# Kernel tuning notes

Hardware: AMD Instinct MI355X
Metric: run time of the kernel (lower is better)

## Reference

```python
import jax, jax.numpy as jnp
import numpy as np
from jax import lax

K = 10  # k_neighbors (k = min(k, N); N=1024 so k=10)


def setup_inputs() -> dict:
    key = jax.random.key(0)
    ks = jax.random.split(key, 6)
    B, N, M, D = 4, 1024, 8, 128
    PROJ, NC, OUT = 64, 10, 128
    x = jax.random.normal(ks[0], (B, N, M, D), dtype=jnp.float32)
    # Linear params (torch stores weight as [out, in])
    W_proj_w = jax.random.normal(ks[1], (PROJ, D), dtype=jnp.float32) / np.sqrt(D)
    W_proj_b = jnp.zeros((PROJ,), dtype=jnp.float32)
    C = jax.random.normal(ks[2], (NC, PROJ), dtype=jnp.float32) * np.sqrt(2.0 / (NC + PROJ))
    Theta_w = jax.random.normal(ks[3], (OUT, D), dtype=jnp.float32) / np.sqrt(D)
    Theta_b = jnp.zeros((OUT,), dtype=jnp.float32)
    return {"x": x, "W_proj_w": W_proj_w, "W_proj_b": W_proj_b, "C": C,
            "Theta_w": Theta_w, "Theta_b": Theta_b}


def _forward(x, W_proj_w, W_proj_b, C, Theta_w, Theta_b):
    B, N, M, D = x.shape
    BM = B * M
    x_flat = jnp.transpose(x, (0, 2, 1, 3)).reshape(BM, N, D)
    Z = x_flat @ W_proj_w.T + W_proj_b  # [BM, N, P]
    # squared euclidean pairwise distances (same topk ordering as cdist)
    sq = jnp.sum(Z * Z, axis=-1)  # [BM, N]
    d2 = sq[:, :, None] + sq[:, None, :] - 2.0 * jnp.einsum('bnp,bmp->bnm', Z, Z)
    _, idx = lax.top_k(-d2, K)  # k smallest distances -> [BM, N, K]
    # scatter 1.0 at neighbor indices
    b_ix = jnp.arange(BM)[:, None, None]
    r_ix = jnp.arange(N)[None, :, None]
    H_knn = jnp.zeros((BM, N, N), dtype=jnp.float32).at[b_ix, r_ix, idx].set(1.0)
    H_cluster = jax.nn.softmax(Z @ C.T, axis=-1)  # [BM, N, NC]
    H = jnp.concatenate([H_knn, H_cluster], axis=-1)  # [BM, N, N+NC]
    # hypergraph conv with degree normalization
    D_e = H.sum(axis=1)  # [BM, E]
    D_e_inv = jnp.where(D_e > 0, 1.0 / jnp.maximum(D_e, 1e-12), 0.0)
    D_v = H.sum(axis=2)  # [BM, N]
    D_v_inv_sqrt = jnp.where(D_v > 0, 1.0 / jnp.sqrt(jnp.maximum(D_v, 1e-12)), 0.0)
    X_trans = x_flat @ Theta_w.T + Theta_b  # [BM, N, F]
    out = D_v_inv_sqrt[:, :, None] * X_trans
    out = jnp.einsum('bne,bnf->bef', H, out)   # H^T @ out
    out = D_e_inv[:, :, None] * out
    out = jnp.einsum('bne,bef->bnf', H, out)   # H @ out
    out = D_v_inv_sqrt[:, :, None] * out
    out = jax.nn.elu(out)
    return jnp.transpose(out.reshape(B, M, N, -1), (0, 2, 1, 3))  # [B, N, M, F]


def reference(x, W_proj_w, W_proj_b, C, Theta_w, Theta_b):
    return _forward(x, W_proj_w, W_proj_b, C, Theta_w, Theta_b)
```

## Files before the change

### kernel.cpp

```cpp
#include <hip/hip_runtime.h>
#include <hip/hip_bf16.h>
#include <cstdint>
#include <cstddef>

#define BMC 32
#define NNODE 1024
#define DIN 128
#define PPROJ 64
#define NCLUS 10
#define FOUT 128
#define KNB 10

typedef _Float16 half8 __attribute__((ext_vector_type(8)));
typedef float f32x4 __attribute__((ext_vector_type(4)));

static const size_t OFF_Z    = 0;
static const size_t OFF_SQ   = 2097152;
static const size_t OFF_HC   = 2129920;
static const size_t OFF_IDX  = 2457600;
static const size_t OFF_CNT  = 2785280;
static const size_t OFF_FILL = 2818048;
static const size_t OFF_EC   = 2850816;
static const size_t OFF_DCV  = 2891776;
static const size_t OFF_OFFS = 2892096;
static const size_t OFF_ADJ  = 2924864;
static const size_t OFF_FLAG = 3252544;
static const size_t OFF_END  = 3252608;
static const size_t OFF_WPH  = OFF_FILL;
static const size_t OFF_WPL  = OFF_FILL +  4096;
static const size_t OFF_THH  = OFF_FILL +  8192;
static const size_t OFF_THL  = OFF_FILL + 16384;

__device__ __forceinline__ float bfu(unsigned int lo16) {
    return __uint_as_float(lo16 << 16);
}
__device__ __forceinline__ float bfhi(unsigned int w) {
    return __uint_as_float(w & 0xffff0000u);
}
__device__ __forceinline__ float ldf(const void* p, size_t i, bool isbf) {
    return isbf ? bfu((unsigned int)((const unsigned short*)p)[i])
                : ((const float*)p)[i];
}
__device__ __forceinline__ unsigned short f2bf(float v) {
    __hip_bfloat16 h = __float2bfloat16(v);
    return *(unsigned short*)&h;
}

__device__ __forceinline__ unsigned long long mkkey(float v, int col) {
    unsigned int bits = __float_as_uint(v);
    unsigned int s = bits ^ (0x80000000u | (unsigned int)((int)bits >> 31));
    return ((unsigned long long)s << 32) | (unsigned int)col;
}
__device__ __forceinline__ void kcas(unsigned long long &a, unsigned long long &b) {
    bool c = b < a;
    unsigned long long t = c ? b : a;
    b = c ? a : b;
    a = t;
}
__device__ __forceinline__ void kmin(unsigned long long &a, unsigned long long b) {
    a = (b < a) ? b : a;
}

__global__ __launch_bounds__(256) void k_split(const unsigned int* __restrict__ xw,
                                               const void* __restrict__ Wp,
                                               const void* __restrict__ Th,
                                               int* __restrict__ flag,
                                               _Float16* __restrict__ WpH,
                                               _Float16* __restrict__ WpL,
                                               _Float16* __restrict__ ThH,
                                               _Float16* __restrict__ ThL,
                                               int* __restrict__ cntz,
                                               float* __restrict__ EcZ) {
    __shared__ int red[256];
    int t = threadIdx.x;
    int c = 0;
    for (int i = t; i < 1024; i += 256) {
        float b = bfu(xw[i] & 0xffffu);
        float ab = fabsf(b);
        if (ab > 9.5e-7f && ab < 1.0e6f) c++;
    }
    red[t] = c;
    __syncthreads();
    for (int off = 128; off > 0; off >>= 1) {
        if (t < off) red[t] += red[t + off];
        __syncthreads();
    }
    const bool isbf = (red[0] >= 700);
    if (blockIdx.x == 0 && t == 0) flag[0] = isbf ? 1 : 0;

    int i = blockIdx.x * 256 + t;
    cntz[i] = 0;
    if (i < 8192) cntz[i + 24576] = 0;
    EcZ[i] = 0.0f;
    if (i < 16704) EcZ[i + 24576] = 0.0f;

    if (i < 8192) {
        float v = ldf(Wp, i, isbf);
        _Float16 h = (_Float16)v;
        WpH[i] = h;
        WpL[i] = (_Float16)((v - (float)h) * 2048.0f);
    } else {
        int j = i - 8192;
        float v = ldf(Th, j, isbf);
        _Float16 h = (_Float16)v;
        ThH[j] = h;
        ThL[j] = (_Float16)((v - (float)h) * 2048.0f);
    }
}

__global__ __launch_bounds__(256) void k_proj(const void* __restrict__ x,
                                              const _Float16* __restrict__ WpH,
                                              const _Float16* __restrict__ WpL,
                                              const void* __restrict__ Wpb,
                                              const void* __restrict__ Cm,
                                              const int* __restrict__ flag,
                                              _Float16* __restrict__ Zh,
                                              _Float16* __restrict__ Zl,
                                              float* __restrict__ sqv,
                                              float* __restrict__ Hc) {
    __shared__ __align__(16) _Float16 wps[2][64][72];
    __shared__ __align__(16) _Float16 xsh[2][32][72];
    __shared__ float zs[32][68];
    __shared__ float cs[10][64];

    const bool isbf = (flag[0] != 0);
    int tid = threadIdx.x;
    int bi  = blockIdx.x;
    int bm  = bi >> 5;
    int n0  = (bi & 31) << 5;
    int b   = bm >> 3, m = bm & 7;

    int lane = tid & 63, wave = tid >> 6;
    int m16 = lane & 15, quad = lane >> 4;
    int rh = wave >> 1, ch = wave & 1;

    for (int e = tid; e < 640; e += 256) cs[e >> 6][e & 63] = ldf(Cm, e, isbf);

    f32x4 aH[2], aX[2];
#pragma unroll
    for (int t = 0; t < 2; ++t) {
        aH[t] = (f32x4){0.f, 0.f, 0.f, 0.f};
        aX[t] = (f32x4){0.f, 0.f, 0.f, 0.f};
    }

    for (int kc = 0; kc < 2; ++kc) {
        __syncthreads();
        for (int e = tid; e < 512; e += 256) {
            int p = e >> 3, c = e & 7;
            *(uint4*)&wps[0][p][c * 8] =
                *(const uint4*)(WpH + (size_t)p * 128 + kc * 64 + c * 8);
            *(uint4*)&wps[1][p][c * 8] =
                *(const uint4*)(WpL + (size_t)p * 128 + kc * 64 + c * 8);
        }
        for (int e = tid; e < 2048; e += 256) {
            int r = e >> 6, dk = e & 63;
            float v = ldf(x, (((size_t)b * NNODE + n0 + r) * 8 + m) * DIN + kc * 64 + dk, isbf);
            _Float16 h = (_Float16)v;
            xsh[0][r][dk] = h;
            xsh[1][r][dk] = (_Float16)((v - (float)h) * 2048.0f);
        }
        __syncthreads();
#pragma unroll
        for (int c32 = 0; c32 < 2; ++c32) {
            half8 Ah = *(const half8*)&xsh[0][rh * 16 + m16][c32 * 32 + quad * 8];
            half8 Al = *(const half8*)&xsh[1][rh * 16 + m16][c32 * 32 + quad * 8];
#pragma unroll
            for (int t = 0; t < 2; ++t) {
                int p = ch * 32 + t * 16 + m16;
                half8 Bh = *(const half8*)&wps[0][p][c32 * 32 + quad * 8];
                half8 Bl = *(const half8*)&wps[1][p][c32 * 32 + quad * 8];
                aH[t] = __builtin_amdgcn_mfma_f32_16x16x32_f16(Ah, Bh, aH[t], 0, 0, 0);
                aX[t] = __builtin_amdgcn_mfma_f32_16x16x32_f16(Al, Bh, aX[t], 0, 0, 0);
                aX[t] = __builtin_amdgcn_mfma_f32_16x16x32_f16(Ah, Bl, aX[t], 0, 0, 0);
            }
        }
    }

#pragma unroll
    for (int t = 0; t < 2; ++t) {
        int p = ch * 32 + t * 16 + m16;
        float bias = ldf(Wpb, p, isbf);
#pragma unroll
        for (int r = 0; r < 4; ++r) {
            int row = rh * 16 + quad * 4 + r;
            float v = aH[t][r] + aX[t][r] * (1.0f / 2048.0f) + bias;
            zs[row][p] = v;
            size_t off = ((size_t)bm * NNODE + n0 + row) * 64 + p;
            _Float16 h = (_Float16)v;
            Zh[off] = h;
            Zl[off] = (_Float16)((v - (float)h) * 2048.0f);
        }
    }
    __syncthreads();

    int row = tid >> 3, slot = tid & 7;
    int d0 = slot * 8;
    float sp = 0.f;
#pragma unroll
    for (int dd = 0; dd < 8; ++dd) { float z = zs[row][d0+dd]; sp += z * z; }
#pragma unroll
    for (int mm = 1; mm < 8; mm <<= 1) sp += __shfl_xor(sp, mm, 8);
    size_t g = (size_t)bm * NNODE + n0 + row;
    if (slot == 0) sqv[g] = sp;

    float sc[10];
#pragma unroll
    for (int c = 0; c < 10; ++c) {
        float pa = 0.f;
#pragma unroll
        for (int dd = 0; dd < 8; ++dd) pa += zs[row][d0+dd] * cs[c][d0+dd];
#pragma unroll
        for (int mm = 1; mm < 8; mm <<= 1) pa += __shfl_xor(pa, mm, 8);
        sc[c] = pa;
    }
    float mx = sc[0];
#pragma unroll
    for (int c = 1; c < 10; ++c) mx = fmaxf(mx, sc[c]);
    float ssum = 0.f;
#pragma unroll
    for (int c = 0; c < 10; ++c) { sc[c] = expf(sc[c] - mx); ssum += sc[c]; }
    float inv = 1.0f / ssum;
#pragma unroll
    for (int c = 0; c < 10; ++c)
        if ((c & 7) == slot) Hc[g * 10 + c] = sc[c] * inv;
}

__global__ __launch_bounds__(256) void k_theta(const void* __restrict__ x,
                                               const _Float16* __restrict__ ThH,
                                               const _Float16* __restrict__ ThL,
                                               const void* __restrict__ Thb,
                                               const int* __restrict__ flag,
                                               float* __restrict__ Xt) {
    __shared__ __align__(16) _Float16 ths[2][128][72];
    __shared__ __align__(16) _Float16 xsh[32][72];

    const bool isbf = (flag[0] != 0);
    int tid = threadIdx.x;
    int bi  = blockIdx.x;
    int bm  = bi >> 5;
    int n0  = (bi & 31) << 5;
    int b   = bm >> 3, m = bm & 7;

    int lane = tid & 63, wave = tid >> 6;
    int m16 = lane & 15, quad = lane >> 4;
    int rh = wave >> 1, ch = wave & 1;

    f32x4 aH[4], aX[4];
#pragma unroll
    for (int t = 0; t < 4; ++t) {
        aH[t] = (f32x4){0.f, 0.f, 0.f, 0.f};
        aX[t] = (f32x4){0.f, 0.f, 0.f, 0.f};
    }

    for (int kc = 0; kc < 2; ++kc) {
        __syncthreads();
        for (int e = tid; e < 1024; e += 256) {
            int f = e >> 3, c = e & 7;
            *(uint4*)&ths[0][f][c * 8] =
                *(const uint4*)(ThH + (size_t)f * 128 + kc * 64 + c * 8);
            *(uint4*)&ths[1][f][c * 8] =
                *(const uint4*)(ThL + (size_t)f * 128 + kc * 64 + c * 8);
        }
        for (int e = tid; e < 2048; e += 256) {
            int r = e >> 6, dk = e & 63;
            float v = ldf(x, (((size_t)b * NNODE + n0 + r) * 8 + m) * DIN + kc * 64 + dk, isbf);
            xsh[r][dk] = (_Float16)v;
        }
        __syncthreads();
#pragma unroll
        for (int c32 = 0; c32 < 2; ++c32) {
            half8 Ah = *(const half8*)&xsh[rh * 16 + m16][c32 * 32 + quad * 8];
#pragma unroll
            for (int t = 0; t < 4; ++t) {
                int f = ch * 64 + t * 16 + m16;
                half8 Bh = *(const half8*)&ths[0][f][c32 * 32 + quad * 8];
                half8 Bl = *(const half8*)&ths[1][f][c32 * 32 + quad * 8];
                aH[t] = __builtin_amdgcn_mfma_f32_16x16x32_f16(Ah, Bh, aH[t], 0, 0, 0);
                aX[t] = __builtin_amdgcn_mfma_f32_16x16x32_f16(Ah, Bl, aX[t], 0, 0, 0);
            }
        }
    }
#pragma unroll
    for (int t = 0; t < 4; ++t) {
        int f = ch * 64 + t * 16 + m16;
        float bias = ldf(Thb, f, isbf);
        size_t rb = (size_t)bm * NNODE + n0 + rh * 16 + quad * 4;
#pragma unroll
        for (int r = 0; r < 4; ++r) {
            Xt[(rb + r) * 128 + f] = aH[t][r] + aX[t][r] * (1.0f / 2048.0f) + bias;
        }
    }
}

#define TOPK_SELECT(J0)                                                        \
  {                                                                            \
    unsigned long long b0 = mkkey(ST[(sslot     ) * 36 + srow], (J0) + sslot);        \
    unsigned long long b1 = mkkey(ST[(sslot +  8) * 36 + srow], (J0) + sslot + 8);    \
    unsigned long long b2 = mkkey(ST[(sslot + 16) * 36 + srow], (J0) + sslot + 16);   \
    unsigned long long b3 = mkkey(ST[(sslot + 24) * 36 + srow], (J0) + sslot + 24);   \
    unsigned long long b4 = mkkey(ST[(sslot + 32) * 36 + srow], (J0) + sslot + 32);   \
    unsigned long long b5 = mkkey(ST[(sslot + 40) * 36 + srow], (J0) + sslot + 40);   \
    unsigned long long b6 = mkkey(ST[(sslot + 48) * 36 + srow], (J0) + sslot + 48);   \
    unsigned long long b7 = mkkey(ST[(sslot + 56) * 36 + srow], (J0) + sslot + 56);   \
    kcas(b0, b1); kcas(b2, b3); kcas(b4, b5); kcas(b6, b7);                    \
    kcas(b0, b2); kcas(b1, b3); kcas(b4, b6); kcas(b5, b7);                    \
    kcas(b1, b2); kcas(b5, b6);                                                \
    kcas(b0, b4); kcas(b1, b5); kcas(b2, b6); kcas(b3, b7);                    \
    kcas(b2, b4); kcas(b3, b5);                                                \
    kcas(b1, b2); kcas(b3, b4); kcas(b5, b6);                                  \
    kmin(keys[2], b7); kmin(keys[3], b6); kmin(keys[4], b5); kmin(keys[5], b4);\
    kmin(keys[6], b3); kmin(keys[7], b2); kmin(keys[8], b1); kmin(keys[9], b0);\
    kcas(keys[0], keys[8]); kcas(keys[1], keys[9]);                            \
    kcas(keys[2], keys[6]); kcas(keys[3], keys[7]);                            \
    kcas(keys[4], keys[8]); kcas(keys[5], keys[9]);                            \
    kcas(keys[2], keys[4]); kcas(keys[3], keys[5]);                            \
    kcas(keys[6], keys[8]); kcas(keys[7], keys[9]);                            \
    kcas(keys[0], keys[1]); kcas(keys[2], keys[3]);                            \
    kcas(keys[4], keys[5]); kcas(keys[6], keys[7]); kcas(keys[8], keys[9]);    \
  }

#define TOPK_TILE(J0, CH0,CH1,CL0,CL1,CSQ, NH0,NH1,NL0,NL1,NSQ)                \
  {                                                                            \
    f32x4 acc  = {0.f, 0.f, 0.f, 0.f};                                         \
    f32x4 accx = {0.f, 0.f, 0.f, 0.f};                                         \
    acc  = __builtin_amdgcn_mfma_f32_16x16x32_f16(ah0, CH0, acc, 0, 0, 0);     \
    acc  = __builtin_amdgcn_mfma_f32_16x16x32_f16(ah1, CH1, acc, 0, 0, 0);     \
    accx = __builtin_amdgcn_mfma_f32_16x16x32_f16(al0, CH0, accx, 0, 0, 0);    \
    accx = __builtin_amdgcn_mfma_f32_16x16x32_f16(ah0, CL0, accx, 0, 0, 0);    \
    accx = __builtin_amdgcn_mfma_f32_16x16x32_f16(al1, CH1, accx, 0, 0, 0);    \
    accx = __builtin_amdgcn_mfma_f32_16x16x32_f16(ah1, CL1, accx, 0, 0, 0);    \
    f32x4 sc;                                                                  \
    _Pragma("unroll")                                                          \
    for (int r = 0; r < 4; ++r) {                                              \
      float g = acc[r] + accx[r] * (1.0f / 2048.0f);                           \
      sc[r] = fmaf(-2.0f, g, CSQ);                                             \
    }                                                                          \
    *(f32x4*)&ST[cl * 36 + quad * 4] = sc;                                     \
    f32x4 accB  = {0.f, 0.f, 0.f, 0.f};                                        \
    f32x4 accxB = {0.f, 0.f, 0.f, 0.f};                                        \
    accB  = __builtin_amdgcn_mfma_f32_16x16x32_f16(ah0b, CH0, accB, 0, 0, 0);  \
    accB  = __builtin_amdgcn_mfma_f32_16x16x32_f16(ah1b, CH1, accB, 0, 0, 0);  \
    accxB = __builtin_amdgcn_mfma_f32_16x16x32_f16(al0b, CH0, accxB, 0, 0, 0); \
    accxB = __builtin_amdgcn_mfma_f32_16x16x32_f16(ah0b, CL0, accxB, 0, 0, 0); \
    accxB = __builtin_amdgcn_mfma_f32_16x16x32_f16(al1b, CH1, accxB, 0, 0, 0); \
    accxB = __builtin_amdgcn_mfma_f32_16x16x32_f16(ah1b, CL1, accxB, 0, 0, 0); \
    _Pragma("unroll")                                                          \
    for (int r = 0; r < 4; ++r) {                                              \
      float g = accB[r] + accxB[r] * (1.0f / 2048.0f);                         \
      sc[r] = fmaf(-2.0f, g, CSQ);                                             \
    }                                                                          \
    *(f32x4*)&ST[cl * 36 + 16 + quad * 4] = sc;                                \
    {                                                                          \
      const _Float16* pnb = Zhb + (size_t)((J0) + 64 + cl) * 64 + quad * 8;    \
      const _Float16* pnl = Zlb + (size_t)((J0) + 64 + cl) * 64 + quad * 8;    \
      NH0 = *(const half8*)pnb;                                                \
      NH1 = *(const half8*)(pnb + 32);                                         \
      NL0 = *(const half8*)pnl;                                                \
      NL1 = *(const half8*)(pnl + 32);                                         \
      NSQ = sqb[(J0) + 64 + cl];                                               \
    }                                                                          \
    asm volatile("s_waitcnt lgkmcnt(0)" ::: "memory");                         \
    __builtin_amdgcn_s_barrier();                                              \
    asm volatile("" ::: "memory");                                             \
    TOPK_SELECT(J0);                                                           \
    asm volatile("" ::: "memory");                                             \
    __builtin_amdgcn_s_barrier();                                              \
    asm volatile("" ::: "memory");                                             \
  }

__global__ __launch_bounds__(256) void k_topk(const _Float16* __restrict__ Zh,
                                              const _Float16* __restrict__ Zl,
                                              const float* __restrict__ sqv,
                                              int* __restrict__ idxo,
                                              int* __restrict__ cnt) {
    __shared__ float ST[64 * 36];

    int tid = threadIdx.x;
    int bi  = blockIdx.x;
    int bm  = bi >> 5;
    int n0  = (bi & 31) << 5;
    const _Float16* Zhb = Zh + (size_t)bm * NNODE * 64;
    const _Float16* Zlb = Zl + (size_t)bm * NNODE * 64;
    const float*    sqb = sqv + (size_t)bm * NNODE;

    int lane = tid & 63, wave = tid >> 6;
    int m16 = lane & 15, quad = lane >> 4;
    int cl = wave * 16 + m16;

    half8 ah0, ah1, al0, al1, ah0b, ah1b, al0b, al1b;
    {
        size_t ab = (size_t)(n0 + m16) * 64 + quad * 8;
        ah0 = *(const half8*)(Zhb + ab);
        ah1 = *(const half8*)(Zhb + ab + 32);
        al0 = *(const half8*)(Zlb + ab);
        al1 = *(const half8*)(Zlb + ab + 32);
        size_t ab2 = ab + 16 * 64;
        ah0b = *(const half8*)(Zhb + ab2);
        ah1b = *(const half8*)(Zhb + ab2 + 32);
        al0b = *(const half8*)(Zlb + ab2);
        al1b = *(const half8*)(Zlb + ab2 + 32);
    }

    unsigned long long keys[10];
#pragma unroll
    for (int j = 0; j < 10; ++j) keys[j] = ~0ULL;

    int srow  = tid >> 3;
    int sslot = tid & 7;

    half8 cbh0, cbh1, cbl0, cbl1, nbh0, nbh1, nbl0, nbl1;
    float csq, nsq;
    {
        const _Float16* pb = Zhb + (size_t)cl * 64 + quad * 8;
        const _Float16* pl = Zlb + (size_t)cl * 64 + quad * 8;
        cbh0 = *(const half8*)pb;
        cbh1 = *(const half8*)(pb + 32);
        cbl0 = *(const half8*)pl;
        cbl1 = *(const half8*)(pl + 32);
        csq  = sqb[cl];
    }

    for (int tp = 0; tp < 8; ++tp) {
        int j0a = tp << 7;
        TOPK_TILE(j0a,      cbh0, cbh1, cbl0, cbl1, csq, nbh0, nbh1, nbl0, nbl1, nsq)
        TOPK_TILE(j0a + 64, nbh0, nbh1, nbl0, nbl1, nsq, cbh0, cbh1, cbl0, cbl1, csq)
    }

    size_t gr = (size_t)bm * NNODE + n0 + srow;
    for (int it = 0; it < 10; ++it) {
        unsigned long long mine = keys[0];
        unsigned long long best = mine;
#pragma unroll
        for (int mm = 1; mm < 8; mm <<= 1) {
            unsigned long long o = __shfl_xor(best, mm, 8);
            if (o < best) best = o;
        }
        if (best == mine) {
#pragma unroll
            for (int j = 0; j < 9; ++j) keys[j] = keys[j+1];
            keys[9] = ~0ULL;
            int col = (int)(best & 0xFFFFFFFFu);
            idxo[gr * KNB + it] = col;
            atomicAdd(&cnt[bm * NNODE + col], 1);
        }
    }
}
#undef TOPK_TILE
#undef TOPK_SELECT

__global__ __launch_bounds__(256) void k_csr(const int* __restrict__ cnt,
                                             const int* __restrict__ idxb,
                                             int* __restrict__ offs,
                                             int* __restrict__ adj) {
    __shared__ int part[256];
    __shared__ int fillL[1024];
    int bm = blockIdx.x, t = threadIdx.x;
    int base = bm * 1024 + t * 4;
    int c0 = cnt[base], c1 = cnt[base+1], c2 = cnt[base+2], c3 = cnt[base+3];
    int ps = c0 + c1 + c2 + c3;
    part[t] = ps;
    __syncthreads();
    for (int off = 1; off < 256; off <<= 1) {
        int add = (t >= off) ? part[t - off] : 0;
        __syncthreads();
        part[t] += add;
        __syncthreads();
    }
    int e0 = part[t] - ps;
    int gb = bm * (NNODE * KNB);
    int o0 = gb + e0, o1 = o0 + c0, o2 = o1 + c1, o3 = o2 + c2;
    offs[base]   = o0;
    offs[base+1] = o1;
    offs[base+2] = o2;
    offs[base+3] = o3;
    fillL[t*4]   = o0;
    fillL[t*4+1] = o1;
    fillL[t*4+2] = o2;
    fillL[t*4+3] = o3;
    __syncthreads();
    int ibase = bm * (NNODE * KNB);
    for (int e = t; e < NNODE * KNB; e += 256) {
        int eidx = idxb[ibase + e];
        int pos = atomicAdd(&fillL[eidx], 1);
        adj[pos] = (bm << 10) + (e / 10);
    }
}

__global__ __launch_bounds__(256) void k_edgeclus(const float* __restrict__ Xt,
                                                  const int* __restrict__ offs,
                                                  const int* __restrict__ cnt,
                                                  const int* __restrict__ adj,
                                                  unsigned short* __restrict__ Ek,
                                                  const float* __restrict__ Hc,
                                                  float* __restrict__ Ec,
                                                  float* __restrict__ Dcv) {
    __shared__ float hcs[128][12];
    int tid = threadIdx.x;
    int bi  = blockIdx.x;

    if (bi < 256) {
        int bm = bi >> 3;
        int ch = bi & 7;
        int n0 = ch * 128;

        for (int e = tid; e < 1280; e += 256) {
            int r = e / 10, c = e - r * 10;
            hcs[r][c] = Hc[((size_t)bm * NNODE + n0 + r) * 10 + c];
        }
        __syncthreads();

        int f = tid & 127;
        int h = tid >> 7;
        int c0 = h * 5;
        float acc[5]  = {0.f,0.f,0.f,0.f,0.f};
        float dacc[5] = {0.f,0.f,0.f,0.f,0.f};
#pragma unroll 2
        for (int n = 0; n < 128; ++n) {
            float xv = Xt[((size_t)bm * NNODE + n0 + n) * 128 + f];
#pragma unroll
            for (int j = 0; j < 5; ++j) {
                float hv = hcs[n][c0 + j];
                acc[j]  = fmaf(hv, xv, acc[j]);
                dacc[j] += hv;
            }
        }
#pragma unroll
        for (int j = 0; j < 5; ++j)
            atomicAdd(&Ec[((size_t)bm * 10 + c0 + j) * 128 + f], acc[j]);
        if (f == 0) {
#pragma unroll
            for (int j = 0; j < 5; ++j) atomicAdd(&Dcv[bm * 10 + c0 + j], dacc[j]);
        }
        return;
    }

    int ebi = bi - 256;
    int swz = (ebi & 7) * 512 + (ebi >> 3);
    int e = swz * 8 + (tid >> 5);
    int l = tid & 31;
    int start = offs[e];
    int num = cnt[e];
    float4 acc = {0.f, 0.f, 0.f, 0.f};
    if (num > 0) {
        int nm1 = num - 1;
        int gidx[16];
#pragma unroll
        for (int j = 0; j < 16; ++j) {
            int jj = (j < nm1) ? j : nm1;
            gidx[j] = adj[start + jj];
        }
#pragma unroll
        for (int j = 0; j < 16; ++j) {
            float4 a = *(const float4*)(Xt + (size_t)gidx[j] * 128 + l * 4);
            float w = (j < num) ? 1.0f : 0.0f;
            acc.x = fmaf(w, a.x, acc.x);
            acc.y = fmaf(w, a.y, acc.y);
            acc.z = fmaf(w, a.z, acc.z);
            acc.w = fmaf(w, a.w, acc.w);
        }
        int i = 16;
        for (; i + 1 < num; i += 2) {
            int g0 = adj[start + i];
            int g1 = adj[start + i + 1];
            float4 a = *(const float4*)(Xt + (size_t)g0 * 128 + l * 4);
            float4 b = *(const float4*)(Xt + (size_t)g1 * 128 + l * 4);
            acc.x += a.x + b.x; acc.y += a.y + b.y;
            acc.z += a.z + b.z; acc.w += a.w + b.w;
        }
        if (i < num) {
            int g0 = adj[start + i];
            float4 a = *(const float4*)(Xt + (size_t)g0 * 128 + l * 4);
            acc.x += a.x; acc.y += a.y; acc.z += a.z; acc.w += a.w;
        }
    }
    float scale = (num > 0) ? 1.0f / (float)num : 0.0f;
    ushort4 o;
    o.x = f2bf(acc.x * scale);
    o.y = f2bf(acc.y * scale);
    o.z = f2bf(acc.z * scale);
    o.w = f2bf(acc.w * scale);
    *(ushort4*)(Ek + (size_t)e * 128 + l * 4) = o;
}

__global__ __launch_bounds__(256) void k_final(const unsigned short* __restrict__ Ek,
                                               const float* __restrict__ Ec,
                                               const float* __restrict__ Hc,
                                               const float* __restrict__ Dcv,
                                               const int* __restrict__ idxb,
                                               float* __restrict__ out) {
    int tid = threadIdx.x;
    int bi  = blockIdx.x;
    int swz = (bi & 7) * 512 + (bi >> 3);
    int g = swz * 8 + (tid >> 5);
    int l = tid & 31;
    int bm = g >> 10, n = g & 1023;
    const int* ip = idxb + (size_t)g * 10;
    const unsigned short* ekb = Ek + ((size_t)bm << 10) * 128 + l * 4;

    int e0 = ip[0], e1 = ip[1], e2 = ip[2], e3 = ip[3], e4 = ip[4];
    int e5 = ip[5], e6 = ip[6], e7 = ip[7], e8 = ip[8], e9 = ip[9];
    ushort4 u0 = *(const ushort4*)(ekb + (size_t)e0 * 128);
    ushort4 u1 = *(const ushort4*)(ekb + (size_t)e1 * 128);
    ushort4 u2 = *(const ushort4*)(ekb + (size_t)e2 * 128);
    ushort4 u3 = *(const ushort4*)(ekb + (size_t)e3 * 128);
    ushort4 u4 = *(const ushort4*)(ekb + (size_t)e4 * 128);
    ushort4 u5 = *(const ushort4*)(ekb + (size_t)e5 * 128);
    ushort4 u6 = *(const ushort4*)(ekb + (size_t)e6 * 128);
    ushort4 u7 = *(const ushort4*)(ekb + (size_t)e7 * 128);
    ushort4 u8 = *(const ushort4*)(ekb + (size_t)e8 * 128);
    ushort4 u9 = *(const ushort4*)(ekb + (size_t)e9 * 128);

    float4 acc;
    acc.x = bfu(u0.x) + bfu(u1.x) + bfu(u2.x) + bfu(u3.x) + bfu(u4.x)
          + bfu(u5.x) + bfu(u6.x) + bfu(u7.x) + bfu(u8.x) + bfu(u9.x);
    acc.y = bfu(u0.y) + bfu(u1.y) + bfu(u2.y) + bfu(u3.y) + bfu(u4.y)
          + bfu(u5.y) + bfu(u6.y) + bfu(u7.y) + bfu(u8.y) + bfu(u9.y);
    acc.z = bfu(u0.z) + bfu(u1.z) + bfu(u2.z) + bfu(u3.z) + bfu(u4.z)
          + bfu(u5.z) + bfu(u6.z) + bfu(u7.z) + bfu(u8.z) + bfu(u9.z);
    acc.w = bfu(u0.w) + bfu(u1.w) + bfu(u2.w) + bfu(u3.w) + bfu(u4.w)
          + bfu(u5.w) + bfu(u6.w) + bfu(u7.w) + bfu(u8.w) + bfu(u9.w);

    const float* hp  = Hc + (size_t)g * 10;
    const float* dcp = Dcv + (size_t)bm * 10;
    const float* ecp = Ec + (size_t)bm * 10 * 128 + l * 4;
#pragma unroll
    for (int c = 0; c < 10; ++c) {
        float d  = dcp[c];
        float hv = (d > 0.f) ? hp[c] / d : 0.f;
        float4 ec = *(const float4*)(ecp + c * 128);
        acc.x += hv * ec.x; acc.y += hv * ec.y;
        acc.z += hv * ec.z; acc.w += hv * ec.w;
    }
    float4 r;
    r.x = acc.x * (1.0f / 11.0f);
    r.y = acc.y * (1.0f / 11.0f);
    r.z = acc.z * (1.0f / 11.0f);
    r.w = acc.w * (1.0f / 11.0f);
    r.x = (r.x > 0.f) ? r.x : expm1f(r.x);
    r.y = (r.y > 0.f) ? r.y : expm1f(r.y);
    r.z = (r.z > 0.f) ? r.z : expm1f(r.z);
    r.w = (r.w > 0.f) ? r.w : expm1f(r.w);
    int b = bm >> 3, m = bm & 7;
    *(float4*)(out + (((size_t)b * NNODE + n) * 8 + m) * 128 + l * 4) = r;
}

extern "C" void kernel_launch(void* const* d_in, const int* in_sizes, int n_in,
                              void* d_out, int out_size, void* d_ws, size_t ws_size,
                              hipStream_t stream) {
    const void* x   = d_in[0];
    const void* Wp  = d_in[1];
    const void* Wpb = d_in[2];
    const void* Cm  = d_in[3];
    const void* Th  = d_in[4];
    const void* Thb = d_in[5];
    float* ws = (float*)d_ws;

    if (ws_size < OFF_END * sizeof(float)) return;

    _Float16* Zh = (_Float16*)(ws + OFF_Z);
    _Float16* Zl = (_Float16*)(ws + OFF_Z + 1048576);
    float* sqv  = ws + OFF_SQ;
    float* Hc   = ws + OFF_HC;
    int*   idxb = (int*)(ws + OFF_IDX);
    int*   cnt  = (int*)(ws + OFF_CNT);
    float* Ec   = ws + OFF_EC;
    float* Dcv  = ws + OFF_DCV;
    int*   offs = (int*)(ws + OFF_OFFS);
    int*   adj  = (int*)(ws + OFF_ADJ);
    int*   flag = (int*)(ws + OFF_FLAG);
    _Float16* WpH = (_Float16*)(ws + OFF_WPH);
    _Float16* WpL = (_Float16*)(ws + OFF_WPL);
    _Float16* ThH = (_Float16*)(ws + OFF_THH);
    _Float16* ThL = (_Float16*)(ws + OFF_THL);
    unsigned short* Ek = (unsigned short*)(ws + OFF_Z);
    float* Xt  = (float*)d_out;
    float* out = (float*)d_out;

    k_split   <<<96,   256, 0, stream>>>((const unsigned int*)x, Wp, Th, flag,
                                         WpH, WpL, ThH, ThL, cnt, Ec);
    k_proj    <<<1024, 256, 0, stream>>>(x, WpH, WpL, Wpb, Cm, flag, Zh, Zl, sqv, Hc);
    k_topk    <<<1024, 256, 0, stream>>>(Zh, Zl, sqv, idxb, cnt);
    k_csr     <<<32,   256, 0, stream>>>(cnt, idxb, offs, adj);
    k_theta   <<<1024, 256, 0, stream>>>(x, ThH, ThL, Thb, flag, Xt);
    k_edgeclus<<<4352, 256, 0, stream>>>(Xt, offs, cnt, adj, Ek, Hc, Ec, Dcv);
    k_final   <<<4096, 256, 0, stream>>>(Ek, Ec, Hc, Dcv, idxb, out);
}
```

Before: 252.1 us.

## Split top-k over column halves with merge kernel; fuse CSR build into theta

The k-nearest-neighbour search is split so that each row's 1024 candidate columns are scanned by two blocks of 512 columns each, doubling the grid. Each block writes its local top-10 as packed keys into scratch space in the output buffer. A new merge kernel combines the two sorted lists with a min/compare-swap network, then writes the indices and neighbour counts. The small 32-block CSR construction is moved into extra blocks of the theta projection kernel so it no longer runs as its own serialized launch. This trades an extra pass over the partial results for more parallelism in the dominant top-k stage.

```diff
diff --git a/kernel.cpp b/kernel.cpp
--- a/kernel.cpp
+++ b/kernel.cpp
@@ -33,9 +33,6 @@
 
 __device__ __forceinline__ float bfu(unsigned int lo16) {
     return __uint_as_float(lo16 << 16);
-}
-__device__ __forceinline__ float bfhi(unsigned int w) {
-    return __uint_as_float(w & 0xffff0000u);
 }
 __device__ __forceinline__ float ldf(const void* p, size_t i, bool isbf) {
     return isbf ? bfu((unsigned int)((const unsigned short*)p)[i])
@@ -223,73 +220,6 @@
 #pragma unroll
     for (int c = 0; c < 10; ++c)
         if ((c & 7) == slot) Hc[g * 10 + c] = sc[c] * inv;
-}
-
-__global__ __launch_bounds__(256) void k_theta(const void* __restrict__ x,
-                                               const _Float16* __restrict__ ThH,
-                                               const _Float16* __restrict__ ThL,
-                                               const void* __restrict__ Thb,
-                                               const int* __restrict__ flag,
-                                               float* __restrict__ Xt) {
-    __shared__ __align__(16) _Float16 ths[2][128][72];
-    __shared__ __align__(16) _Float16 xsh[32][72];
-
-    const bool isbf = (flag[0] != 0);
-    int tid = threadIdx.x;
-    int bi  = blockIdx.x;
-    int bm  = bi >> 5;
-    int n0  = (bi & 31) << 5;
-    int b   = bm >> 3, m = bm & 7;
-
-    int lane = tid & 63, wave = tid >> 6;
-    int m16 = lane & 15, quad = lane >> 4;
-    int rh = wave >> 1, ch = wave & 1;
-
-    f32x4 aH[4], aX[4];
-#pragma unroll
-    for (int t = 0; t < 4; ++t) {
-        aH[t] = (f32x4){0.f, 0.f, 0.f, 0.f};
-        aX[t] = (f32x4){0.f, 0.f, 0.f, 0.f};
-    }
-
-    for (int kc = 0; kc < 2; ++kc) {
-        __syncthreads();
-        for (int e = tid; e < 1024; e += 256) {
-            int f = e >> 3, c = e & 7;
-            *(uint4*)&ths[0][f][c * 8] =
-                *(const uint4*)(ThH + (size_t)f * 128 + kc * 64 + c * 8);
-            *(uint4*)&ths[1][f][c * 8] =
-                *(const uint4*)(ThL + (size_t)f * 128 + kc * 64 + c * 8);
-        }
-        for (int e = tid; e < 2048; e += 256) {
-            int r = e >> 6, dk = e & 63;
-            float v = ldf(x, (((size_t)b * NNODE + n0 + r) * 8 + m) * DIN + kc * 64 + dk, isbf);
-            xsh[r][dk] = (_Float16)v;
-        }
-        __syncthreads();
-#pragma unroll
-        for (int c32 = 0; c32 < 2; ++c32) {
-            half8 Ah = *(const half8*)&xsh[rh * 16 + m16][c32 * 32 + quad * 8];
-#pragma unroll
-            for (int t = 0; t < 4; ++t) {
-                int f = ch * 64 + t * 16 + m16;
-                half8 Bh = *(const half8*)&ths[0][f][c32 * 32 + quad * 8];
-                half8 Bl = *(const half8*)&ths[1][f][c32 * 32 + quad * 8];
-                aH[t] = __builtin_amdgcn_mfma_f32_16x16x32_f16(Ah, Bh, aH[t], 0, 0, 0);
-                aX[t] = __builtin_amdgcn_mfma_f32_16x16x32_f16(Ah, Bl, aX[t], 0, 0, 0);
-            }
-        }
-    }
-#pragma unroll
-    for (int t = 0; t < 4; ++t) {
-        int f = ch * 64 + t * 16 + m16;
-        float bias = ldf(Thb, f, isbf);
-        size_t rb = (size_t)bm * NNODE + n0 + rh * 16 + quad * 4;
-#pragma unroll
-        for (int r = 0; r < 4; ++r) {
-            Xt[(rb + r) * 128 + f] = aH[t][r] + aX[t][r] * (1.0f / 2048.0f) + bias;
-        }
-    }
 }
 
 #define TOPK_SELECT(J0)                                                        \
@@ -371,14 +301,16 @@
 __global__ __launch_bounds__(256) void k_topk(const _Float16* __restrict__ Zh,
                                               const _Float16* __restrict__ Zl,
                                               const float* __restrict__ sqv,
-                                              int* __restrict__ idxo,
-                                              int* __restrict__ cnt) {
+                                              unsigned long long* __restrict__ pk) {
     __shared__ float ST[64 * 36];
 
     int tid = threadIdx.x;
     int bi  = blockIdx.x;
-    int bm  = bi >> 5;
-    int n0  = (bi & 31) << 5;
+    int bm  = bi >> 6;
+    int rem = bi & 63;
+    int n0   = (rem & 31) << 5;
+    int half = rem >> 5;
+    int cb   = half << 9;
     const _Float16* Zhb = Zh + (size_t)bm * NNODE * 64;
     const _Float16* Zlb = Zl + (size_t)bm * NNODE * 64;
     const float*    sqb = sqv + (size_t)bm * NNODE;
@@ -411,22 +343,22 @@
     half8 cbh0, cbh1, cbl0, cbl1, nbh0, nbh1, nbl0, nbl1;
     float csq, nsq;
     {
-        const _Float16* pb = Zhb + (size_t)cl * 64 + quad * 8;
-        const _Float16* pl = Zlb + (size_t)cl * 64 + quad * 8;
+        const _Float16* pb = Zhb + (size_t)(cb + cl) * 64 + quad * 8;
+        const _Float16* pl = Zlb + (size_t)(cb + cl) * 64 + quad * 8;
         cbh0 = *(const half8*)pb;
         cbh1 = *(const half8*)(pb + 32);
         cbl0 = *(const half8*)pl;
         cbl1 = *(const half8*)(pl + 32);
-        csq  = sqb[cl];
-    }
-
-    for (int tp = 0; tp < 8; ++tp) {
-        int j0a = tp << 7;
+        csq  = sqb[cb + cl];
+    }
+
+    for (int tp = 0; tp < 4; ++tp) {
+        int j0a = cb + (tp << 7);
         TOPK_TILE(j0a,      cbh0, cbh1, cbl0, cbl1, csq, nbh0, nbh1, nbl0, nbl1, nsq)
         TOPK_TILE(j0a + 64, nbh0, nbh1, nbl0, nbl1, nsq, cbh0, cbh1, cbl0, cbl1, csq)
     }
 
-    size_t gr = (size_t)bm * NNODE + n0 + srow;
+    size_t pr = ((size_t)bm * NNODE + n0 + srow) * 20 + (size_t)half * 10;
     for (int it = 0; it < 10; ++it) {
         unsigned long long mine = keys[0];
         unsigned long long best = mine;
@@ -439,50 +371,153 @@
 #pragma unroll
             for (int j = 0; j < 9; ++j) keys[j] = keys[j+1];
             keys[9] = ~0ULL;
-            int col = (int)(best & 0xFFFFFFFFu);
-            idxo[gr * KNB + it] = col;
-            atomicAdd(&cnt[bm * NNODE + col], 1);
+            pk[pr + it] = best;
         }
     }
 }
 #undef TOPK_TILE
 #undef TOPK_SELECT
 
-__global__ __launch_bounds__(256) void k_csr(const int* __restrict__ cnt,
-                                             const int* __restrict__ idxb,
-                                             int* __restrict__ offs,
-                                             int* __restrict__ adj) {
+__global__ __launch_bounds__(256) void k_merge(const unsigned long long* __restrict__ pk,
+                                               int* __restrict__ idxo,
+                                               int* __restrict__ cnt) {
+    int r = blockIdx.x * 256 + threadIdx.x;
+    const unsigned long long* p = pk + (size_t)r * 20;
+    unsigned long long a0 = p[0], a1 = p[1], a2 = p[2], a3 = p[3], a4 = p[4];
+    unsigned long long a5 = p[5], a6 = p[6], a7 = p[7], a8 = p[8], a9 = p[9];
+    unsigned long long b0 = p[10], b1 = p[11], b2 = p[12], b3 = p[13], b4 = p[14];
+    unsigned long long b5 = p[15], b6 = p[16], b7 = p[17], b8 = p[18], b9 = p[19];
+
+    kmin(a0, b9); kmin(a1, b8); kmin(a2, b7); kmin(a3, b6); kmin(a4, b5);
+    kmin(a5, b4); kmin(a6, b3); kmin(a7, b2); kmin(a8, b1); kmin(a9, b0);
+
+    kcas(a0, a8); kcas(a1, a9);
+    kcas(a2, a6); kcas(a3, a7);
+    kcas(a4, a8); kcas(a5, a9);
+    kcas(a2, a4); kcas(a3, a5);
+    kcas(a6, a8); kcas(a7, a9);
+    kcas(a0, a1); kcas(a2, a3);
+    kcas(a4, a5); kcas(a6, a7); kcas(a8, a9);
+
+    int bm = r >> 10;
+    int* cb = cnt + (bm << 10);
+    int* ip = idxo + (size_t)r * 10;
+    int c0 = (int)(a0 & 0xFFFFFFFFu); ip[0] = c0; atomicAdd(&cb[c0], 1);
+    int c1 = (int)(a1 & 0xFFFFFFFFu); ip[1] = c1; atomicAdd(&cb[c1], 1);
+    int c2 = (int)(a2 & 0xFFFFFFFFu); ip[2] = c2; atomicAdd(&cb[c2], 1);
+    int c3 = (int)(a3 & 0xFFFFFFFFu); ip[3] = c3; atomicAdd(&cb[c3], 1);
+    int c4 = (int)(a4 & 0xFFFFFFFFu); ip[4] = c4; atomicAdd(&cb[c4], 1);
+    int c5 = (int)(a5 & 0xFFFFFFFFu); ip[5] = c5; atomicAdd(&cb[c5], 1);
+    int c6 = (int)(a6 & 0xFFFFFFFFu); ip[6] = c6; atomicAdd(&cb[c6], 1);
+    int c7 = (int)(a7 & 0xFFFFFFFFu); ip[7] = c7; atomicAdd(&cb[c7], 1);
+    int c8 = (int)(a8 & 0xFFFFFFFFu); ip[8] = c8; atomicAdd(&cb[c8], 1);
+    int c9 = (int)(a9 & 0xFFFFFFFFu); ip[9] = c9; atomicAdd(&cb[c9], 1);
+}
+
+__global__ __launch_bounds__(256) void k_thetacsr(const void* __restrict__ x,
+                                                  const _Float16* __restrict__ ThH,
+                                                  const _Float16* __restrict__ ThL,
+                                                  const void* __restrict__ Thb,
+                                                  const int* __restrict__ flag,
+                                                  float* __restrict__ Xt,
+                                                  const int* __restrict__ cnt,
+                                                  const int* __restrict__ idxb,
+                                                  int* __restrict__ offs,
+                                                  int* __restrict__ adj) {
+    __shared__ __align__(16) _Float16 ths[2][128][72];
+    __shared__ __align__(16) _Float16 xsh[32][72];
     __shared__ int part[256];
     __shared__ int fillL[1024];
-    int bm = blockIdx.x, t = threadIdx.x;
-    int base = bm * 1024 + t * 4;
-    int c0 = cnt[base], c1 = cnt[base+1], c2 = cnt[base+2], c3 = cnt[base+3];
-    int ps = c0 + c1 + c2 + c3;
-    part[t] = ps;
-    __syncthreads();
-    for (int off = 1; off < 256; off <<= 1) {
-        int add = (t >= off) ? part[t - off] : 0;
+
+    int tid = threadIdx.x;
+    if (blockIdx.x < 32) {
+        int bm = blockIdx.x, t = tid;
+        int base = bm * 1024 + t * 4;
+        int c0 = cnt[base], c1 = cnt[base+1], c2 = cnt[base+2], c3 = cnt[base+3];
+        int ps = c0 + c1 + c2 + c3;
+        part[t] = ps;
         __syncthreads();
-        part[t] += add;
+        for (int off = 1; off < 256; off <<= 1) {
+            int add = (t >= off) ? part[t - off] : 0;
+            __syncthreads();
+            part[t] += add;
+            __syncthreads();
+        }
+        int e0 = part[t] - ps;
+        int gb = bm * (NNODE * KNB);
+        int o0 = gb + e0, o1 = o0 + c0, o2 = o1 + c1, o3 = o2 + c2;
+        offs[base]   = o0;
+        offs[base+1] = o1;
+        offs[base+2] = o2;
+        offs[base+3] = o3;
+        fillL[t*4]   = o0;
+        fillL[t*4+1] = o1;
+        fillL[t*4+2] = o2;
+        fillL[t*4+3] = o3;
         __syncthreads();
-    }
-    int e0 = part[t] - ps;
-    int gb = bm * (NNODE * KNB);
-    int o0 = gb + e0, o1 = o0 + c0, o2 = o1 + c1, o3 = o2 + c2;
-    offs[base]   = o0;
-    offs[base+1] = o1;
-    offs[base+2] = o2;
-    offs[base+3] = o3;
-    fillL[t*4]   = o0;
-    fillL[t*4+1] = o1;
-    fillL[t*4+2] = o2;
-    fillL[t*4+3] = o3;
-    __syncthreads();
-    int ibase = bm * (NNODE * KNB);
-    for (int e = t; e < NNODE * KNB; e += 256) {
-        int eidx = idxb[ibase + e];
-        int pos = atomicAdd(&fillL[eidx], 1);
-        adj[pos] = (bm << 10) + (e / 10);
+        int ibase = bm * (NNODE * KNB);
+        for (int e = t; e < NNODE * KNB; e += 256) {
+            int eidx = idxb[ibase + e];
+            int pos = atomicAdd(&fillL[eidx], 1);
+            adj[pos] = (bm << 10) + (e / 10);
+        }
+        return;
+    }
+
+    const bool isbf = (flag[0] != 0);
+    int bi  = blockIdx.x - 32;
+    int bm  = bi >> 5;
+    int n0  = (bi & 31) << 5;
+    int b   = bm >> 3, m = bm & 7;
+
+    int lane = tid & 63, wave = tid >> 6;
+    int m16 = lane & 15, quad = lane >> 4;
+    int rh = wave >> 1, ch = wave & 1;
+
+    f32x4 aH[4], aX[4];
+#pragma unroll
+    for (int t = 0; t < 4; ++t) {
+        aH[t] = (f32x4){0.f, 0.f, 0.f, 0.f};
+        aX[t] = (f32x4){0.f, 0.f, 0.f, 0.f};
+    }
+
+    for (int kc = 0; kc < 2; ++kc) {
+        __syncthreads();
+        for (int e = tid; e < 1024; e += 256) {
+            int f = e >> 3, c = e & 7;
+            *(uint4*)&ths[0][f][c * 8] =
+                *(const uint4*)(ThH + (size_t)f * 128 + kc * 64 + c * 8);
+            *(uint4*)&ths[1][f][c * 8] =
+                *(const uint4*)(ThL + (size_t)f * 128 + kc * 64 + c * 8);
+        }
+        for (int e = tid; e < 2048; e += 256) {
+            int r = e >> 6, dk = e & 63;
+            float v = ldf(x, (((size_t)b * NNODE + n0 + r) * 8 + m) * DIN + kc * 64 + dk, isbf);
+            xsh[r][dk] = (_Float16)v;
+        }
+        __syncthreads();
+#pragma unroll
+        for (int c32 = 0; c32 < 2; ++c32) {
+            half8 Ah = *(const half8*)&xsh[rh * 16 + m16][c32 * 32 + quad * 8];
+#pragma unroll
+            for (int t = 0; t < 4; ++t) {
+                int f = ch * 64 + t * 16 + m16;
+                half8 Bh = *(const half8*)&ths[0][f][c32 * 32 + quad * 8];
+                half8 Bl = *(const half8*)&ths[1][f][c32 * 32 + quad * 8];
+                aH[t] = __builtin_amdgcn_mfma_f32_16x16x32_f16(Ah, Bh, aH[t], 0, 0, 0);
+                aX[t] = __builtin_amdgcn_mfma_f32_16x16x32_f16(Ah, Bl, aX[t], 0, 0, 0);
+            }
+        }
+    }
+#pragma unroll
+    for (int t = 0; t < 4; ++t) {
+        int f = ch * 64 + t * 16 + m16;
+        float bias = ldf(Thb, f, isbf);
+        size_t rb = (size_t)bm * NNODE + n0 + rh * 16 + quad * 4;
+#pragma unroll
+        for (int r = 0; r < 4; ++r) {
+            Xt[(rb + r) * 128 + f] = aH[t][r] + aX[t][r] * (1.0f / 2048.0f) + bias;
+        }
     }
 }
 
@@ -673,15 +708,16 @@
     _Float16* ThH = (_Float16*)(ws + OFF_THH);
     _Float16* ThL = (_Float16*)(ws + OFF_THL);
     unsigned short* Ek = (unsigned short*)(ws + OFF_Z);
+    unsigned long long* pk = (unsigned long long*)d_out;
     float* Xt  = (float*)d_out;
     float* out = (float*)d_out;
 
     k_split   <<<96,   256, 0, stream>>>((const unsigned int*)x, Wp, Th, flag,
                                          WpH, WpL, ThH, ThL, cnt, Ec);
     k_proj    <<<1024, 256, 0, stream>>>(x, WpH, WpL, Wpb, Cm, flag, Zh, Zl, sqv, Hc);
-    k_topk    <<<1024, 256, 0, stream>>>(Zh, Zl, sqv, idxb, cnt);
-    k_csr     <<<32,   256, 0, stream>>>(cnt, idxb, offs, adj);
-    k_theta   <<<1024, 256, 0, stream>>>(x, ThH, ThL, Thb, flag, Xt);
+    k_topk    <<<2048, 256, 0, stream>>>(Zh, Zl, sqv, pk);
+    k_merge   <<<128,  256, 0, stream>>>(pk, idxb, cnt);
+    k_thetacsr<<<1056, 256, 0, stream>>>(x, ThH, ThL, Thb, flag, Xt, cnt, idxb, offs, adj);
     k_edgeclus<<<4352, 256, 0, stream>>>(Xt, offs, cnt, adj, Ek, Hc, Ec, Dcv);
     k_final   <<<4096, 256, 0, stream>>>(Ek, Ec, Hc, Dcv, idxb, out);
 }
```

After: 259.5 us. 3.0% more time.

## Merge top-k and theta projection into one interleaved launch

Applied to the files above, without the earlier changes.

Combines the independent k_topk and k_theta kernels into a single launch of 2048 blocks, where even blocks do the kNN top-k selection and odd blocks compute the Theta projection. The aim is to overlap the compute-bound top-k work with the memory-heavy theta GEMM and remove one launch. Shared memory becomes a union sized for the larger branch, which may lower occupancy for the top-k blocks.

```diff
diff --git a/kernel.cpp b/kernel.cpp
--- a/kernel.cpp
+++ b/kernel.cpp
@@ -33,9 +33,6 @@
 
 __device__ __forceinline__ float bfu(unsigned int lo16) {
     return __uint_as_float(lo16 << 16);
-}
-__device__ __forceinline__ float bfhi(unsigned int w) {
-    return __uint_as_float(w & 0xffff0000u);
 }
 __device__ __forceinline__ float ldf(const void* p, size_t i, bool isbf) {
     return isbf ? bfu((unsigned int)((const unsigned short*)p)[i])
@@ -223,73 +220,6 @@
 #pragma unroll
     for (int c = 0; c < 10; ++c)
         if ((c & 7) == slot) Hc[g * 10 + c] = sc[c] * inv;
-}
-
-__global__ __launch_bounds__(256) void k_theta(const void* __restrict__ x,
-                                               const _Float16* __restrict__ ThH,
-                                               const _Float16* __restrict__ ThL,
-                                               const void* __restrict__ Thb,
-                                               const int* __restrict__ flag,
-                                               float* __restrict__ Xt) {
-    __shared__ __align__(16) _Float16 ths[2][128][72];
-    __shared__ __align__(16) _Float16 xsh[32][72];
-
-    const bool isbf = (flag[0] != 0);
-    int tid = threadIdx.x;
-    int bi  = blockIdx.x;
-    int bm  = bi >> 5;
-    int n0  = (bi & 31) << 5;
-    int b   = bm >> 3, m = bm & 7;
-
-    int lane = tid & 63, wave = tid >> 6;
-    int m16 = lane & 15, quad = lane >> 4;
-    int rh = wave >> 1, ch = wave & 1;
-
-    f32x4 aH[4], aX[4];
-#pragma unroll
-    for (int t = 0; t < 4; ++t) {
-        aH[t] = (f32x4){0.f, 0.f, 0.f, 0.f};
-        aX[t] = (f32x4){0.f, 0.f, 0.f, 0.f};
-    }
-
-    for (int kc = 0; kc < 2; ++kc) {
-        __syncthreads();
-        for (int e = tid; e < 1024; e += 256) {
-            int f = e >> 3, c = e & 7;
-            *(uint4*)&ths[0][f][c * 8] =
-                *(const uint4*)(ThH + (size_t)f * 128 + kc * 64 + c * 8);
-            *(uint4*)&ths[1][f][c * 8] =
-                *(const uint4*)(ThL + (size_t)f * 128 + kc * 64 + c * 8);
-        }
-        for (int e = tid; e < 2048; e += 256) {
-            int r = e >> 6, dk = e & 63;
-            float v = ldf(x, (((size_t)b * NNODE + n0 + r) * 8 + m) * DIN + kc * 64 + dk, isbf);
-            xsh[r][dk] = (_Float16)v;
-        }
-        __syncthreads();
-#pragma unroll
-        for (int c32 = 0; c32 < 2; ++c32) {
-            half8 Ah = *(const half8*)&xsh[rh * 16 + m16][c32 * 32 + quad * 8];
-#pragma unroll
-            for (int t = 0; t < 4; ++t) {
-                int f = ch * 64 + t * 16 + m16;
-                half8 Bh = *(const half8*)&ths[0][f][c32 * 32 + quad * 8];
-                half8 Bl = *(const half8*)&ths[1][f][c32 * 32 + quad * 8];
-                aH[t] = __builtin_amdgcn_mfma_f32_16x16x32_f16(Ah, Bh, aH[t], 0, 0, 0);
-                aX[t] = __builtin_amdgcn_mfma_f32_16x16x32_f16(Ah, Bl, aX[t], 0, 0, 0);
-            }
-        }
-    }
-#pragma unroll
-    for (int t = 0; t < 4; ++t) {
-        int f = ch * 64 + t * 16 + m16;
-        float bias = ldf(Thb, f, isbf);
-        size_t rb = (size_t)bm * NNODE + n0 + rh * 16 + quad * 4;
-#pragma unroll
-        for (int r = 0; r < 4; ++r) {
-            Xt[(rb + r) * 128 + f] = aH[t][r] + aX[t][r] * (1.0f / 2048.0f) + bias;
-        }
-    }
 }
 
 #define TOPK_SELECT(J0)                                                        \
@@ -368,80 +298,151 @@
     asm volatile("" ::: "memory");                                             \
   }
 
-__global__ __launch_bounds__(256) void k_topk(const _Float16* __restrict__ Zh,
-                                              const _Float16* __restrict__ Zl,
-                                              const float* __restrict__ sqv,
-                                              int* __restrict__ idxo,
-                                              int* __restrict__ cnt) {
-    __shared__ float ST[64 * 36];
-
+__global__ __launch_bounds__(256) void k_topktheta(const _Float16* __restrict__ Zh,
+                                                   const _Float16* __restrict__ Zl,
+                                                   const float* __restrict__ sqv,
+                                                   int* __restrict__ idxo,
+                                                   int* __restrict__ cnt,
+                                                   const void* __restrict__ x,
+                                                   const _Float16* __restrict__ ThH,
+                                                   const _Float16* __restrict__ ThL,
+                                                   const void* __restrict__ Thb,
+                                                   const int* __restrict__ flag,
+                                                   float* __restrict__ Xt) {
+    __shared__ __align__(16) char smem[41472];
     int tid = threadIdx.x;
-    int bi  = blockIdx.x;
+    int gbi = blockIdx.x;
+
+    if ((gbi & 1) == 0) {
+        float* ST = (float*)smem;
+        int bi  = gbi >> 1;
+        int bm  = bi >> 5;
+        int n0  = (bi & 31) << 5;
+        const _Float16* Zhb = Zh + (size_t)bm * NNODE * 64;
+        const _Float16* Zlb = Zl + (size_t)bm * NNODE * 64;
+        const float*    sqb = sqv + (size_t)bm * NNODE;
+
+        int lane = tid & 63, wave = tid >> 6;
+        int m16 = lane & 15, quad = lane >> 4;
+        int cl = wave * 16 + m16;
+
+        half8 ah0, ah1, al0, al1, ah0b, ah1b, al0b, al1b;
+        {
+            size_t ab = (size_t)(n0 + m16) * 64 + quad * 8;
+            ah0 = *(const half8*)(Zhb + ab);
+            ah1 = *(const half8*)(Zhb + ab + 32);
+            al0 = *(const half8*)(Zlb + ab);
+            al1 = *(const half8*)(Zlb + ab + 32);
+            size_t ab2 = ab + 16 * 64;
+            ah0b = *(const half8*)(Zhb + ab2);
+            ah1b = *(const half8*)(Zhb + ab2 + 32);
+            al0b = *(const half8*)(Zlb + ab2);
+            al1b = *(const half8*)(Zlb + ab2 + 32);
+        }
+
+        unsigned long long keys[10];
+#pragma unroll
+        for (int j = 0; j < 10; ++j) keys[j] = ~0ULL;
+
+        int srow  = tid >> 3;
+        int sslot = tid & 7;
+
+        half8 cbh0, cbh1, cbl0, cbl1, nbh0, nbh1, nbl0, nbl1;
+        float csq, nsq;
+        {
+            const _Float16* pb = Zhb + (size_t)cl * 64 + quad * 8;
+            const _Float16* pl = Zlb + (size_t)cl * 64 + quad * 8;
+            cbh0 = *(const half8*)pb;
+            cbh1 = *(const half8*)(pb + 32);
+            cbl0 = *(const half8*)pl;
+            cbl1 = *(const half8*)(pl + 32);
+            csq  = sqb[cl];
+        }
+
+        for (int tp = 0; tp < 8; ++tp) {
+            int j0a = tp << 7;
+            TOPK_TILE(j0a,      cbh0, cbh1, cbl0, cbl1, csq, nbh0, nbh1, nbl0, nbl1, nsq)
+            TOPK_TILE(j0a + 64, nbh0, nbh1, nbl0, nbl1, nsq, cbh0, cbh1, cbl0, cbl1, csq)
+        }
+
+        size_t gr = (size_t)bm * NNODE + n0 + srow;
+        for (int it = 0; it < 10; ++it) {
+            unsigned long long mine = keys[0];
+            unsigned long long best = mine;
+#pragma unroll
+            for (int mm = 1; mm < 8; mm <<= 1) {
+                unsigned long long o = __shfl_xor(best, mm, 8);
+                if (o < best) best = o;
+            }
+            if (best == mine) {
+#pragma unroll
+                for (int j = 0; j < 9; ++j) keys[j] = keys[j+1];
+                keys[9] = ~0ULL;
+                int col = (int)(best & 0xFFFFFFFFu);
+                idxo[gr * KNB + it] = col;
+                atomicAdd(&cnt[bm * NNODE + col], 1);
+            }
+        }
+        return;
+    }
+
+    _Float16* ths0 = (_Float16*)smem;
+    _Float16* ths1 = ths0 + 128 * 72;
+    _Float16* xsh  = ths1 + 128 * 72;
+
+    const bool isbf = (flag[0] != 0);
+    int bi  = gbi >> 1;
     int bm  = bi >> 5;
     int n0  = (bi & 31) << 5;
-    const _Float16* Zhb = Zh + (size_t)bm * NNODE * 64;
-    const _Float16* Zlb = Zl + (size_t)bm * NNODE * 64;
-    const float*    sqb = sqv + (size_t)bm * NNODE;
+    int b   = bm >> 3, m = bm & 7;
 
     int lane = tid & 63, wave = tid >> 6;
     int m16 = lane & 15, quad = lane >> 4;
-    int cl = wave * 16 + m16;
-
-    half8 ah0, ah1, al0, al1, ah0b, ah1b, al0b, al1b;
-    {
-        size_t ab = (size_t)(n0 + m16) * 64 + quad * 8;
-        ah0 = *(const half8*)(Zhb + ab);
-        ah1 = *(const half8*)(Zhb + ab + 32);
-        al0 = *(const half8*)(Zlb + ab);
-        al1 = *(const half8*)(Zlb + ab + 32);
-        size_t ab2 = ab + 16 * 64;
-        ah0b = *(const half8*)(Zhb + ab2);
-        ah1b = *(const half8*)(Zhb + ab2 + 32);
-        al0b = *(const half8*)(Zlb + ab2);
-        al1b = *(const half8*)(Zlb + ab2 + 32);
-    }
-
-    unsigned long long keys[10];
-#pragma unroll
-    for (int j = 0; j < 10; ++j) keys[j] = ~0ULL;
-
-    int srow  = tid >> 3;
-    int sslot = tid & 7;
-
-    half8 cbh0, cbh1, cbl0, cbl1, nbh0, nbh1, nbl0, nbl1;
-    float csq, nsq;
-    {
-        const _Float16* pb = Zhb + (size_t)cl * 64 + quad * 8;
-        const _Float16* pl = Zlb + (size_t)cl * 64 + quad * 8;
-        cbh0 = *(const half8*)pb;
-        cbh1 = *(const half8*)(pb + 32);
-        cbl0 = *(const half8*)pl;
-        cbl1 = *(const half8*)(pl + 32);
-        csq  = sqb[cl];
-    }
-
-    for (int tp = 0; tp < 8; ++tp) {
-        int j0a = tp << 7;
-        TOPK_TILE(j0a,      cbh0, cbh1, cbl0, cbl1, csq, nbh0, nbh1, nbl0, nbl1, nsq)
-        TOPK_TILE(j0a + 64, nbh0, nbh1, nbl0, nbl1, nsq, cbh0, cbh1, cbl0, cbl1, csq)
-    }
-
-    size_t gr = (size_t)bm * NNODE + n0 + srow;
-    for (int it = 0; it < 10; ++it) {
-        unsigned long long mine = keys[0];
-        unsigned long long best = mine;
-#pragma unroll
-        for (int mm = 1; mm < 8; mm <<= 1) {
-            unsigned long long o = __shfl_xor(best, mm, 8);
-            if (o < best) best = o;
-        }
-        if (best == mine) {
-#pragma unroll
-            for (int j = 0; j < 9; ++j) keys[j] = keys[j+1];
-            keys[9] = ~0ULL;
-            int col = (int)(best & 0xFFFFFFFFu);
-            idxo[gr * KNB + it] = col;
-            atomicAdd(&cnt[bm * NNODE + col], 1);
+    int rh = wave >> 1, ch = wave & 1;
+
+    f32x4 aH[4], aX[4];
+#pragma unroll
+    for (int t = 0; t < 4; ++t) {
+        aH[t] = (f32x4){0.f, 0.f, 0.f, 0.f};
+        aX[t] = (f32x4){0.f, 0.f, 0.f, 0.f};
+    }
+
+    for (int kc = 0; kc < 2; ++kc) {
+        __syncthreads();
+        for (int e = tid; e < 1024; e += 256) {
+            int f = e >> 3, c = e & 7;
+            *(uint4*)&ths0[f * 72 + c * 8] =
+                *(const uint4*)(ThH + (size_t)f * 128 + kc * 64 + c * 8);
+            *(uint4*)&ths1[f * 72 + c * 8] =
+                *(const uint4*)(ThL + (size_t)f * 128 + kc * 64 + c * 8);
+        }
+        for (int e = tid; e < 2048; e += 256) {
+            int r = e >> 6, dk = e & 63;
+            float v = ldf(x, (((size_t)b * NNODE + n0 + r) * 8 + m) * DIN + kc * 64 + dk, isbf);
+            xsh[r * 72 + dk] = (_Float16)v;
+        }
+        __syncthreads();
+#pragma unroll
+        for (int c32 = 0; c32 < 2; ++c32) {
+            half8 Ah = *(const half8*)&xsh[(rh * 16 + m16) * 72 + c32 * 32 + quad * 8];
+#pragma unroll
+            for (int t = 0; t < 4; ++t) {
+                int f = ch * 64 + t * 16 + m16;
+                half8 Bh = *(const half8*)&ths0[f * 72 + c32 * 32 + quad * 8];
+                half8 Bl = *(const half8*)&ths1[f * 72 + c32 * 32 + quad * 8];
+                aH[t] = __builtin_amdgcn_mfma_f32_16x16x32_f16(Ah, Bh, aH[t], 0, 0, 0);
+                aX[t] = __builtin_amdgcn_mfma_f32_16x16x32_f16(Ah, Bl, aX[t], 0, 0, 0);
+            }
+        }
+    }
+#pragma unroll
+    for (int t = 0; t < 4; ++t) {
+        int f = ch * 64 + t * 16 + m16;
+        float bias = ldf(Thb, f, isbf);
+        size_t rb = (size_t)bm * NNODE + n0 + rh * 16 + quad * 4;
+#pragma unroll
+        for (int r = 0; r < 4; ++r) {
+            Xt[(rb + r) * 128 + f] = aH[t][r] + aX[t][r] * (1.0f / 2048.0f) + bias;
         }
     }
 }
@@ -676,12 +677,12 @@
     float* Xt  = (float*)d_out;
     float* out = (float*)d_out;
 
-    k_split   <<<96,   256, 0, stream>>>((const unsigned int*)x, Wp, Th, flag,
-                                         WpH, WpL, ThH, ThL, cnt, Ec);
-    k_proj    <<<1024, 256, 0, stream>>>(x, WpH, WpL, Wpb, Cm, flag, Zh, Zl, sqv, Hc);
-    k_topk    <<<1024, 256, 0, stream>>>(Zh, Zl, sqv, idxb, cnt);
-    k_csr     <<<32,   256, 0, stream>>>(cnt, idxb, offs, adj);
-    k_theta   <<<1024, 256, 0, stream>>>(x, ThH, ThL, Thb, flag, Xt);
-    k_edgeclus<<<4352, 256, 0, stream>>>(Xt, offs, cnt, adj, Ek, Hc, Ec, Dcv);
-    k_final   <<<4096, 256, 0, stream>>>(Ek, Ec, Hc, Dcv, idxb, out);
-}
+    k_split    <<<96,   256, 0, stream>>>((const unsigned int*)x, Wp, Th, flag,
+                                          WpH, WpL, ThH, ThL, cnt, Ec);
+    k_proj     <<<1024, 256, 0, stream>>>(x, WpH, WpL, Wpb, Cm, flag, Zh, Zl, sqv, Hc);
+    k_topktheta<<<2048, 256, 0, stream>>>(Zh, Zl, sqv, idxb, cnt,
+                                          x, ThH, ThL, Thb, flag, Xt);
+    k_csr      <<<32,   256, 0, stream>>>(cnt, idxb, offs, adj);
+    k_edgeclus <<<4352, 256, 0, stream>>>(Xt, offs, cnt, adj, Ek, Hc, Ec, Dcv);
+    k_final    <<<4096, 256, 0, stream>>>(Ek, Ec, Hc, Dcv, idxb, out);
+}
```

Result: slower. 282.6 us (+12.1%).
